# Kernel optimization log

Measured on AMD Instinct MI355X. Metric: run time of the kernel, lower is better.

## Reference

```python
import jax, jax.numpy as jnp
import numpy as np

B, S, H, D = 2, 4096, 16, 128
TILE = 128
T = S // TILE          # 32 tiles
TOPK = 7               # anchor-selected tiles per query tile (local tile appended -> 8)
DM = H * D
NEG = -1e10


def setup_inputs() -> dict:
    key = jax.random.key(0)
    ks = jax.random.split(key, 6)
    x = jax.random.normal(ks[0], (B, S, DM), dtype=jnp.float32)
    wq = jax.random.normal(ks[1], (DM, H * D), dtype=jnp.float32) * 0.02
    wk = jax.random.normal(ks[2], (DM, H * D), dtype=jnp.float32) * 0.02
    wv = jax.random.normal(ks[3], (DM, H * D), dtype=jnp.float32) * 0.02
    wo = jax.random.normal(ks[4], (H * D, DM), dtype=jnp.float32) * 0.02
    # RoPE tables (real/imag of freqs_cis), LLaMA-style
    inv_freq = 1.0 / (10000.0 ** (np.arange(0, D, 2, dtype=np.float32) / D))  # [D/2]
    t = np.arange(S, dtype=np.float32)
    freqs = np.outer(t, inv_freq)  # [S, D/2]
    cos = jnp.asarray(np.cos(freqs), dtype=jnp.float32)
    sin = jnp.asarray(np.sin(freqs), dtype=jnp.float32)
    anchor_indices = jax.random.randint(ks[5], (B, H, T, TOPK), 0, T, dtype=jnp.int32)
    return {"x": x, "wq": wq, "wk": wk, "wv": wv, "wo": wo,
            "cos": cos, "sin": sin, "anchor_indices": anchor_indices}


def _apply_rope(q, k, cos, sin):
    # q,k: [B,H,S,D]; cos,sin: [S,D/2]
    cos_f = jnp.concatenate([cos, cos], axis=-1)[None, None]  # [1,1,S,D]
    sin_f = jnp.concatenate([sin, sin], axis=-1)[None, None]

    def rot_half(x):
        h = x.shape[-1] // 2
        return jnp.concatenate([-x[..., h:], x[..., :h]], axis=-1)

    return q * cos_f + rot_half(q) * sin_f, k * cos_f + rot_half(k) * sin_f


def reference(x, wq, wk, wv, wo, cos, sin, anchor_indices):
    b, s, _ = x.shape
    h = anchor_indices.shape[1]
    t = anchor_indices.shape[2]
    tile = s // t
    d = wq.shape[1] // h

    q = (x @ wq).reshape(b, s, h, d).transpose(0, 2, 1, 3)  # [B,H,S,D]
    k = (x @ wk).reshape(b, s, h, d).transpose(0, 2, 1, 3)
    v = (x @ wv).reshape(b, s, h, d).transpose(0, 2, 1, 3)
    q, k = _apply_rope(q, k, cos, sin)

    # append local tile to anchor-selected tiles -> [B,H,T,K+1]
    local = jnp.broadcast_to(jnp.arange(t, dtype=jnp.int32)[None, None, :, None], (b, h, t, 1))
    tile_sel = jnp.concatenate([anchor_indices, local], axis=-1)
    # token indices of gathered tiles: [B,H,T,(K+1)*tile]
    offs = jnp.arange(tile, dtype=jnp.int32)[None, None, None, None, :]
    tok_idx = (tile_sel[..., None] * tile + offs)
    sparse_len = tile_sel.shape[-1] * tile
    flat_idx = jnp.clip(tok_idx.reshape(b, h, t, sparse_len), 0, s - 1)

    # gather K/V tiles: [B,H,T,L,D]
    gid = flat_idx.reshape(b, h, t * sparse_len)
    k_sp = jnp.take_along_axis(k, gid[..., None], axis=2).reshape(b, h, t, sparse_len, d)
    v_sp = jnp.take_along_axis(v, gid[..., None], axis=2).reshape(b, h, t, sparse_len, d)

    q_t = q.reshape(b, h, t, tile, d)
    logits = jnp.einsum('bhtqd,bhtkd->bhtqk', q_t, k_sp) / jnp.sqrt(jnp.float32(d))

    # causal future-mask within gathered set
    q_pos = jnp.arange(s, dtype=jnp.int32).reshape(t, tile)
    fut = flat_idx[:, :, :, None, :] > q_pos[None, None, :, :, None]  # [B,H,T,tile,L]
    logits = jnp.where(fut, NEG, logits)
    weights = jax.nn.softmax(logits, axis=-1)
    all_masked = jnp.all(fut, axis=-1, keepdims=True)
    weights = jnp.where(all_masked, 0.0, weights)
    weights = jnp.where(jnp.isnan(weights), 0.0, weights)

    out = jnp.einsum('bhtqk,bhtkd->bhtqd', weights, v_sp)
    out = out.reshape(b, h, s, d).transpose(0, 2, 1, 3).reshape(b, s, h * d)
    return out @ wo
```

## Files before the change

### kernel.cpp

```cpp
#include <hip/hip_runtime.h>
#include <hip/hip_bf16.h>


typedef __bf16 bf16_t;
using bf16x8 = __attribute__((ext_vector_type(8))) __bf16;
using bf16x4 = __attribute__((ext_vector_type(4))) __bf16;
using f32x4  = __attribute__((ext_vector_type(4))) float;

typedef const __attribute__((address_space(1))) void* gas_ptr;
typedef __attribute__((address_space(3))) void* las_ptr;

__device__ __forceinline__ void async_copy16(const void* g, void* l) {
  __builtin_amdgcn_global_load_lds((gas_ptr)g, (las_ptr)l, 16, 0, 0);
}

__device__ __forceinline__ f32x4 mfma16x16x32(bf16x8 a, bf16x8 b, f32x4 c) {
  return __builtin_amdgcn_mfma_f32_16x16x32_bf16(a, b, c, 0, 0, 0);
}

__global__ void cvt_f32_bf16(const float* __restrict__ X, bf16_t* __restrict__ Y) {
  int idx = blockIdx.x * 256 + threadIdx.x;
  float4 v = ((const float4*)X)[idx];
  bf16x4 r;
  r.x = (bf16_t)v.x; r.y = (bf16_t)v.y; r.z = (bf16_t)v.z; r.w = (bf16_t)v.w;
  ((bf16x4*)Y)[idx] = r;
}

__global__ void wtrans(const float* __restrict__ W, bf16_t* __restrict__ Wt) {
  __shared__ bf16_t t[64][66];
  const int r0 = blockIdx.x * 64, c0 = blockIdx.y * 64;
  const int tx = threadIdx.x & 63, ty = threadIdx.x >> 6;
  #pragma unroll
  for (int i = 0; i < 16; ++i) {
    int r = ty + 4 * i;
    t[r][tx] = (bf16_t)W[(size_t)(r0 + r) * 2048 + c0 + tx];
  }
  __syncthreads();
  #pragma unroll
  for (int i = 0; i < 16; ++i) {
    int n = ty + 4 * i;
    Wt[(size_t)(c0 + n) * 2048 + r0 + tx] = t[tx][n];
  }
}

__global__ __launch_bounds__(512, 2) void gemm256(
    const bf16_t* __restrict__ A, const bf16_t* __restrict__ Bt,
    int nb, int mode, float* __restrict__ Cf,
    bf16_t* __restrict__ outQ, bf16_t* __restrict__ outK,
    bf16_t* __restrict__ outVT,
    const float* __restrict__ cosT, const float* __restrict__ sinT)
{
  __shared__ bf16_t Apan[4][8192];
  __shared__ bf16_t Bpan[4][8192];
  const int bid = blockIdx.x;
  const int cpx = gridDim.x >> 3;
  const int swz = (bid & 7) * cpx + (bid >> 3);
  const int bm = (swz / nb) * 256, bn = (swz % nb) * 256;
  const int tid = threadIdx.x;
  const int w = tid >> 6, l = tid & 63;
  const int wr = w >> 1, wc = w & 1;
  const int fr = l & 15, g4 = l >> 4;

  const int c0 = tid, c1 = tid + 512;
  const int r0 = c0 >> 2, s0c = ((c0 & 3) ^ ((r0 >> 1) & 3)) * 8;
  const int r1 = c1 >> 2, s1c = ((c1 & 3) ^ ((r1 >> 1) & 3)) * 8;
  const bf16_t* aS0 = A  + (size_t)(bm + r0) * 2048 + s0c;
  const bf16_t* aS1 = A  + (size_t)(bm + r1) * 2048 + s1c;
  const bf16_t* bS0 = Bt + (size_t)(bn + r0) * 2048 + s0c;
  const bf16_t* bS1 = Bt + (size_t)(bn + r1) * 2048 + s1c;
  const int d0 = c0 * 16, d1 = c1 * 16;

  int aOff[4], bOff[8];
  #pragma unroll
  for (int m = 0; m < 4; ++m) {
    int R = wr * 64 + m * 16 + fr;
    aOff[m] = R * 64 + ((g4 ^ ((R >> 1) & 3)) << 4);
  }
  #pragma unroll
  for (int n = 0; n < 8; ++n) {
    int R = wc * 128 + n * 16 + fr;
    bOff[n] = R * 64 + ((g4 ^ ((R >> 1) & 3)) << 4);
  }

  f32x4 acc[4][8];
  #pragma unroll
  for (int m = 0; m < 4; ++m)
    #pragma unroll
    for (int n = 0; n < 8; ++n) acc[m][n] = (f32x4){0.f, 0.f, 0.f, 0.f};

  auto STAGE = [&](int phi2) {
    const int slot = phi2 & 3;
    const int kb = phi2 * 32;
    char* dA = (char*)&Apan[slot][0];
    char* dB = (char*)&Bpan[slot][0];
    async_copy16(aS0 + kb, dA + d0);
    async_copy16(aS1 + kb, dA + d1);
    async_copy16(bS0 + kb, dB + d0);
    async_copy16(bS1 + kb, dB + d1);
  };

  STAGE(0);
  STAGE(1);
  __syncthreads();

  #pragma unroll 1
  for (int phi = 0; phi < 64; ++phi) {
    const int slot = phi & 3;
    const char* pa = (const char*)&Apan[slot][0];
    const char* pb = (const char*)&Bpan[slot][0];
    bf16x8 af[4], bfr[8];
    #pragma unroll
    for (int m = 0; m < 4; ++m) af[m] = *(const bf16x8*)(pa + aOff[m]);
    #pragma unroll
    for (int n = 0; n < 8; ++n) bfr[n] = *(const bf16x8*)(pb + bOff[n]);
    if (phi < 62) {
      STAGE(phi + 2);
      asm volatile("s_waitcnt vmcnt(4)" ::: "memory");
    } else {
      asm volatile("s_waitcnt vmcnt(0)" ::: "memory");
    }
    __builtin_amdgcn_sched_barrier(0);
    __builtin_amdgcn_s_barrier();
    __builtin_amdgcn_sched_barrier(0);
    __builtin_amdgcn_s_setprio(1);
    #pragma unroll
    for (int m = 0; m < 4; ++m)
      #pragma unroll
      for (int n = 0; n < 8; ++n)
        acc[m][n] = mfma16x16x32(af[m], bfr[n], acc[m][n]);
    __builtin_amdgcn_s_setprio(0);
    __builtin_amdgcn_sched_barrier(0);
  }

  if (mode == 0) {
    #pragma unroll
    for (int m = 0; m < 4; ++m)
      #pragma unroll
      for (int n = 0; n < 8; ++n)
        #pragma unroll
        for (int j = 0; j < 4; ++j) {
          int row = bm + wr * 64 + m * 16 + g4 * 4 + j;
          int col = bn + wc * 128 + n * 16 + fr;
          Cf[(size_t)row * 2048 + col] = acc[m][n][j];
        }
    return;
  }

  const int colbase = bn + wc * 128;
  const int proj = colbase >> 11;
  const int hh = (colbase & 2047) >> 7;
  if (proj == 2) {
    #pragma unroll
    for (int m = 0; m < 4; ++m) {
      int row0 = bm + wr * 64 + m * 16 + g4 * 4;
      int b_ = row0 >> 12, sr = row0 & 4095;
      #pragma unroll
      for (int n = 0; n < 8; ++n) {
        int d_ = n * 16 + fr;
        bf16x4 pkv;
        #pragma unroll
        for (int j = 0; j < 4; ++j) pkv[j] = (bf16_t)acc[m][n][j];
        *(bf16x4*)&outVT[(((size_t)(b_ * 16 + hh)) * 128 + d_) * 4096 + sr] = pkv;
      }
    }
  } else {
    bf16_t* dst = proj ? outK : outQ;
    #pragma unroll
    for (int m = 0; m < 4; ++m) {
      int row0 = bm + wr * 64 + m * 16 + g4 * 4;
      int b_ = row0 >> 12, s0 = row0 & 4095;
      size_t hbase = ((size_t)(b_ * 16 + hh)) * 4096;
      #pragma unroll
      for (int n = 0; n < 4; ++n) {
        int d = n * 16 + fr;
        #pragma unroll
        for (int j = 0; j < 4; ++j) {
          int s = s0 + j;
          float c  = cosT[s * 64 + d];
          float sn = sinT[s * 64 + d];
          float x0 = acc[m][n][j], x1 = acc[m][n + 4][j];
          dst[(hbase + s) * 128 + d]      = (bf16_t)(x0 * c - x1 * sn);
          dst[(hbase + s) * 128 + d + 64] = (bf16_t)(x1 * c + x0 * sn);
        }
      }
    }
  }
}

__global__ __launch_bounds__(512, 4) void attn_kernel(
    const bf16_t* __restrict__ Qf, const bf16_t* __restrict__ Kf,
    const bf16_t* __restrict__ Vt, const int* __restrict__ anchors,
    bf16_t* __restrict__ outB)
{
  __shared__ bf16_t Kl[2][8192];
  __shared__ bf16_t Vl[2][8192];
  __shared__ bf16_t Pbuf[8][1024];
  const int orig = blockIdx.x;
  const int blk = (orig & 7) * 128 + (orig >> 3);
  const int qt = 31 - (blk & 31);
  const int h = (blk >> 5) & 15, b = blk >> 9;
  const int bh = b * 16 + h;
  const int tid = threadIdx.x, w = tid >> 6, l = tid & 63;
  const int fr = l & 15, g4 = l >> 4;
  const float scale = 0.08838834764831845f;

  const int* anc = anchors + ((size_t)bh * 32 + qt) * 7;
  unsigned long long pk = 0;
  int nt = 0;
  #pragma unroll
  for (int t = 0; t < 7; ++t) {
    int v = anc[t];
    if (v <= qt) { pk |= (unsigned long long)v << (5 * nt); ++nt; }
  }
  pk |= (unsigned long long)qt << (5 * nt); ++nt;
  const int NS = nt * 2;

  const bf16_t* Qbase = Qf + (size_t)bh * 4096 * 128;
  const bf16_t* Kbase = Kf + (size_t)bh * 4096 * 128;
  const bf16_t* Vbase = Vt + (size_t)bh * 128 * 4096;
  char* P = (char*)&Pbuf[w][0];

  auto STAGE = [&](int tb2, int p) {
    const bf16_t* ksrc = Kbase + (size_t)tb2 * 128;
    const bf16_t* vsrc = Vbase + tb2;
    char* kd = (char*)&Kl[p][0];
    char* vd = (char*)&Vl[p][0];
    #pragma unroll
    for (int i = 0; i < 2; ++i) {
      int c = tid + i * 512;
      int kr = c >> 4, kcol = c & 15;
      async_copy16(ksrc + (size_t)kr * 128 + (size_t)((kcol ^ (kr & 7)) * 8),
                   kd + c * 16);
      int vr = c >> 3, vcol = c & 7;
      async_copy16(vsrc + (size_t)vr * 4096 + (size_t)((vcol ^ (vr & 7)) * 8),
                   vd + c * 16);
    }
  };

  const int qrow = qt * 128 + w * 16 + fr;
  bf16x8 aq[4];
  #pragma unroll
  for (int kc = 0; kc < 4; ++kc)
    aq[kc] = *(const bf16x8*)(Qbase + (size_t)qrow * 128 + kc * 32 + g4 * 8);

  STAGE((int)(pk & 31) * 128, 0);
  __syncthreads();

  float mrun = -1e30f, lrun = 0.f;
  f32x4 o[8];
  #pragma unroll
  for (int nd = 0; nd < 8; ++nd) o[nd] = (f32x4){0.f, 0.f, 0.f, 0.f};

  for (int s = 0; s < NS; ++s) {
    const int p = s & 1;
    const int ts = (int)((pk >> (5 * (s >> 1))) & 31);
    const bool domask = (ts == qt);
    if (s + 1 < NS) {
      int s1 = s + 1;
      int ts1 = (int)((pk >> (5 * (s1 >> 1))) & 31);
      STAGE(ts1 * 128 + (s1 & 1) * 64, p ^ 1);
    }

    f32x4 sc[4];
    #pragma unroll
    for (int n = 0; n < 4; ++n) sc[n] = (f32x4){0.f, 0.f, 0.f, 0.f};
    #pragma unroll
    for (int kc = 0; kc < 4; ++kc) {
      bf16x8 kf[4];
      #pragma unroll
      for (int n = 0; n < 4; ++n) {
        int r = n * 16 + fr;
        kf[n] = *(const bf16x8*)((const char*)&Kl[p][0] +
                 r * 256 + (((kc * 4 + g4) ^ (r & 7)) << 4));
      }
      #pragma unroll
      for (int n = 0; n < 4; ++n)
        sc[n] = mfma16x16x32(kf[n], aq[kc], sc[n]);
    }

    float rmax = -1e30f;
    if (domask) {
      const int qr = w * 16 + fr;
      #pragma unroll
      for (int n = 0; n < 4; ++n)
        #pragma unroll
        for (int j = 0; j < 4; ++j) {
          float lg = sc[n][j] * scale;
          int tok = (s & 1) * 64 + n * 16 + g4 * 4 + j;
          if (tok > qr) lg = -1e10f;
          sc[n][j] = lg;
          rmax = fmaxf(rmax, lg);
        }
    } else {
      #pragma unroll
      for (int n = 0; n < 4; ++n)
        #pragma unroll
        for (int j = 0; j < 4; ++j) {
          float lg = sc[n][j] * scale;
          sc[n][j] = lg;
          rmax = fmaxf(rmax, lg);
        }
    }
    rmax = fmaxf(rmax, __shfl_xor(rmax, 16));
    rmax = fmaxf(rmax, __shfl_xor(rmax, 32));
    if (__any(rmax > mrun + 8.f)) {
      float mnew = fmaxf(mrun, rmax);
      float alpha = __expf(mrun - mnew);
      lrun *= alpha;
      #pragma unroll
      for (int nd = 0; nd < 8; ++nd)
        #pragma unroll
        for (int j = 0; j < 4; ++j) o[nd][j] *= alpha;
      mrun = mnew;
    }
    float rsum = 0.f;
    #pragma unroll
    for (int n = 0; n < 4; ++n) {
      bf16x4 pkv;
      #pragma unroll
      for (int j = 0; j < 4; ++j) {
        float pe = __expf(sc[n][j] - mrun);
        rsum += pe;
        pkv[j] = (bf16_t)pe;
      }
      int off = fr * 128 + ((((n << 1) | (g4 >> 1)) ^ (fr & 7)) << 4) + ((g4 & 1) << 3);
      *(bf16x4*)(P + off) = pkv;
    }
    rsum += __shfl_xor(rsum, 16);
    rsum += __shfl_xor(rsum, 32);
    lrun += rsum;

    #pragma unroll
    for (int kc2 = 0; kc2 < 2; ++kc2) {
      bf16x8 av[8];
      #pragma unroll
      for (int nd = 0; nd < 8; ++nd) {
        int r = nd * 16 + fr;
        av[nd] = *(const bf16x8*)((const char*)&Vl[p][0] +
                  r * 128 + (((kc2 * 4 + g4) ^ (r & 7)) << 4));
      }
      bf16x8 bp = *(const bf16x8*)(P + fr * 128 + ((((kc2 << 2) | g4) ^ (fr & 7)) << 4));
      #pragma unroll
      for (int nd = 0; nd < 8; ++nd)
        o[nd] = mfma16x16x32(av[nd], bp, o[nd]);
    }
    __syncthreads();
  }

  {
    char* E = (char*)&Kl[0][0] + w * 4096;
    float inv = 1.0f / lrun;
    #pragma unroll
    for (int nd = 0; nd < 8; ++nd) {
      bf16x4 pkv;
      #pragma unroll
      for (int j = 0; j < 4; ++j) pkv[j] = (bf16_t)(o[nd][j] * inv);
      int off = fr * 256 + ((((nd << 1) | (g4 >> 1)) ^ (fr & 7)) << 4) + ((g4 & 1) << 3);
      *(bf16x4*)(E + off) = pkv;
    }
    #pragma unroll
    for (int i = 0; i < 4; ++i) {
      int r = i * 4 + g4;
      int off = r * 256 + ((fr ^ (r & 7)) << 4);
      bf16x8 vrow = *(const bf16x8*)(E + off);
      size_t gaddr = (((size_t)b * 4096 + qt * 128 + w * 16 + r) * 2048)
                     + h * 128 + fr * 8;
      *(bf16x8*)(outB + gaddr) = vrow;
    }
  }
}

#define OFF_XB   ((size_t)0)
#define OFF_WCAT ((size_t)33554432)
#define OFF_WOT  ((size_t)58720256)
#define OFF_QF   ((size_t)67108864)
#define OFF_KF   ((size_t)100663296)
#define OFF_AT   ((size_t)134217728)
#define OFF_VT   ((size_t)167772160)

extern "C" void kernel_launch(void* const* d_in, const int* in_sizes, int n_in,
                              void* d_out, int out_size, void* d_ws, size_t ws_size,
                              hipStream_t stream) {
  (void)in_sizes; (void)n_in; (void)out_size; (void)ws_size;
  const float* x    = (const float*)d_in[0];
  const float* wq   = (const float*)d_in[1];
  const float* wk   = (const float*)d_in[2];
  const float* wv   = (const float*)d_in[3];
  const float* wo   = (const float*)d_in[4];
  const float* cosT = (const float*)d_in[5];
  const float* sinT = (const float*)d_in[6];
  const int*   anc  = (const int*)d_in[7];
  float* out = (float*)d_out;
  char* ws = (char*)d_ws;

  bf16_t* xb   = (bf16_t*)(ws + OFF_XB);
  bf16_t* wcat = (bf16_t*)(ws + OFF_WCAT);
  bf16_t* wqt  = wcat;
  bf16_t* wkt  = wcat + (size_t)2048 * 2048;
  bf16_t* wvt  = wcat + (size_t)4096 * 2048;
  bf16_t* wot  = (bf16_t*)(ws + OFF_WOT);
  bf16_t* Qf   = (bf16_t*)(ws + OFF_QF);
  bf16_t* Kf   = (bf16_t*)(ws + OFF_KF);
  bf16_t* Vt   = (bf16_t*)(ws + OFF_VT);
  bf16_t* attnB = (bf16_t*)(ws + OFF_AT);

  cvt_f32_bf16<<<16384, 256, 0, stream>>>(x, xb);
  wtrans<<<dim3(32, 32), 256, 0, stream>>>(wq, wqt);
  wtrans<<<dim3(32, 32), 256, 0, stream>>>(wk, wkt);
  wtrans<<<dim3(32, 32), 256, 0, stream>>>(wv, wvt);
  wtrans<<<dim3(32, 32), 256, 0, stream>>>(wo, wot);
  gemm256<<<768, 512, 0, stream>>>(xb, wcat, 24, 1, nullptr, Qf, Kf, Vt, cosT, sinT);
  attn_kernel<<<1024, 512, 0, stream>>>(Qf, Kf, Vt, anc, attnB);
  gemm256<<<256, 512, 0, stream>>>(attnB, wot, 8, 0, out, nullptr, nullptr, nullptr,
                                   nullptr, nullptr);
}
```

Baseline: 382.4 us.

## Split GEMM k-step into four sub-phases interleaving loads, async copies and MFMAs

Each k-iteration of the GEMM main loop is split into four sub-phases. Each sub-phase loads two B fragments, issues one of the four async global-to-LDS copies and runs 8 MFMAs. The aim is to spread LDS reads and global loads across the MFMA work, cut register pressure from holding eight B fragments, and overlap memory with compute more finely. In exchange it adds three extra workgroup barriers per iteration, and the prologue now waits only on the first stage instead of doing a full sync.

```diff
diff --git a/kernel.cpp b/kernel.cpp
--- a/kernel.cpp
+++ b/kernel.cpp
@@ -88,48 +88,55 @@
     #pragma unroll
     for (int n = 0; n < 8; ++n) acc[m][n] = (f32x4){0.f, 0.f, 0.f, 0.f};
 
-  auto STAGE = [&](int phi2) {
+  auto STAGE1 = [&](int phi2, int q) {
     const int slot = phi2 & 3;
     const int kb = phi2 * 32;
-    char* dA = (char*)&Apan[slot][0];
-    char* dB = (char*)&Bpan[slot][0];
-    async_copy16(aS0 + kb, dA + d0);
-    async_copy16(aS1 + kb, dA + d1);
-    async_copy16(bS0 + kb, dB + d0);
-    async_copy16(bS1 + kb, dB + d1);
+    if (q == 0)      async_copy16(aS0 + kb, (char*)&Apan[slot][0] + d0);
+    else if (q == 1) async_copy16(aS1 + kb, (char*)&Apan[slot][0] + d1);
+    else if (q == 2) async_copy16(bS0 + kb, (char*)&Bpan[slot][0] + d0);
+    else             async_copy16(bS1 + kb, (char*)&Bpan[slot][0] + d1);
   };
 
-  STAGE(0);
-  STAGE(1);
-  __syncthreads();
+  #pragma unroll
+  for (int q = 0; q < 4; ++q) STAGE1(0, q);
+  #pragma unroll
+  for (int q = 0; q < 4; ++q) STAGE1(1, q);
+  asm volatile("s_waitcnt vmcnt(4)" ::: "memory");
+  __builtin_amdgcn_sched_barrier(0);
+  __builtin_amdgcn_s_barrier();
+  __builtin_amdgcn_sched_barrier(0);
 
   #pragma unroll 1
   for (int phi = 0; phi < 64; ++phi) {
     const int slot = phi & 3;
     const char* pa = (const char*)&Apan[slot][0];
     const char* pb = (const char*)&Bpan[slot][0];
-    bf16x8 af[4], bfr[8];
-    #pragma unroll
-    for (int m = 0; m < 4; ++m) af[m] = *(const bf16x8*)(pa + aOff[m]);
-    #pragma unroll
-    for (int n = 0; n < 8; ++n) bfr[n] = *(const bf16x8*)(pb + bOff[n]);
-    if (phi < 62) {
-      STAGE(phi + 2);
-      asm volatile("s_waitcnt vmcnt(4)" ::: "memory");
-    } else {
-      asm volatile("s_waitcnt vmcnt(0)" ::: "memory");
-    }
-    __builtin_amdgcn_sched_barrier(0);
-    __builtin_amdgcn_s_barrier();
-    __builtin_amdgcn_sched_barrier(0);
-    __builtin_amdgcn_s_setprio(1);
-    #pragma unroll
-    for (int m = 0; m < 4; ++m)
-      #pragma unroll
-      for (int n = 0; n < 8; ++n)
-        acc[m][n] = mfma16x16x32(af[m], bfr[n], acc[m][n]);
-    __builtin_amdgcn_s_setprio(0);
-    __builtin_amdgcn_sched_barrier(0);
+    bf16x8 af[4];
+    #pragma unroll
+    for (int q = 0; q < 4; ++q) {
+      if (q == 0) {
+        #pragma unroll
+        for (int m = 0; m < 4; ++m) af[m] = *(const bf16x8*)(pa + aOff[m]);
+      }
+      bf16x8 b0 = *(const bf16x8*)(pb + bOff[2 * q]);
+      bf16x8 b1 = *(const bf16x8*)(pb + bOff[2 * q + 1]);
+      if (phi < 62) STAGE1(phi + 2, q);
+      if (q == 3) {
+        if (phi < 62) asm volatile("s_waitcnt vmcnt(4)" ::: "memory");
+        else          asm volatile("s_waitcnt vmcnt(0)" ::: "memory");
+      }
+      __builtin_amdgcn_sched_barrier(0);
+      __builtin_amdgcn_s_barrier();
+      __builtin_amdgcn_sched_barrier(0);
+      __builtin_amdgcn_s_setprio(1);
+      #pragma unroll
+      for (int m = 0; m < 4; ++m) {
+        acc[m][2 * q]     = mfma16x16x32(af[m], b0, acc[m][2 * q]);
+        acc[m][2 * q + 1] = mfma16x16x32(af[m], b1, acc[m][2 * q + 1]);
+      }
+      __builtin_amdgcn_s_setprio(0);
+      __builtin_amdgcn_sched_barrier(0);
+    }
   }
 
   if (mode == 0) {
```

Result: slower. 409.6 us (+7.1%).

## Restructure GEMM K-loop to 64-wide double-buffered stages with one barrier each

Applied to the files above, without the earlier changes.

The GEMM main loop now stages 64-wide K slices into two LDS buffers instead of 32-wide slices into four, with a matching 8-chunk XOR swizzle. Each iteration runs two MFMA sub-steps between barriers, halving barrier count per K. The prefetch depth drops from two stages ahead to one, and each iteration waits on vmcnt(0) after compute. This may expose more global-load latency.

```diff
diff --git a/kernel.cpp b/kernel.cpp
--- a/kernel.cpp
+++ b/kernel.cpp
@@ -50,8 +50,8 @@
     bf16_t* __restrict__ outVT,
     const float* __restrict__ cosT, const float* __restrict__ sinT)
 {
-  __shared__ bf16_t Apan[4][8192];
-  __shared__ bf16_t Bpan[4][8192];
+  __shared__ bf16_t Apan[2][16384];
+  __shared__ bf16_t Bpan[2][16384];
   const int bid = blockIdx.x;
   const int cpx = gridDim.x >> 3;
   const int swz = (bid & 7) * cpx + (bid >> 3);
@@ -61,25 +61,32 @@
   const int wr = w >> 1, wc = w & 1;
   const int fr = l & 15, g4 = l >> 4;
 
-  const int c0 = tid, c1 = tid + 512;
-  const int r0 = c0 >> 2, s0c = ((c0 & 3) ^ ((r0 >> 1) & 3)) * 8;
-  const int r1 = c1 >> 2, s1c = ((c1 & 3) ^ ((r1 >> 1) & 3)) * 8;
-  const bf16_t* aS0 = A  + (size_t)(bm + r0) * 2048 + s0c;
-  const bf16_t* aS1 = A  + (size_t)(bm + r1) * 2048 + s1c;
-  const bf16_t* bS0 = Bt + (size_t)(bn + r0) * 2048 + s0c;
-  const bf16_t* bS1 = Bt + (size_t)(bn + r1) * 2048 + s1c;
-  const int d0 = c0 * 16, d1 = c1 * 16;
-
-  int aOff[4], bOff[8];
-  #pragma unroll
-  for (int m = 0; m < 4; ++m) {
-    int R = wr * 64 + m * 16 + fr;
-    aOff[m] = R * 64 + ((g4 ^ ((R >> 1) & 3)) << 4);
-  }
-  #pragma unroll
-  for (int n = 0; n < 8; ++n) {
-    int R = wc * 128 + n * 16 + fr;
-    bOff[n] = R * 64 + ((g4 ^ ((R >> 1) & 3)) << 4);
+  const bf16_t* aS[4];
+  const bf16_t* bS[4];
+  int dst[4];
+  #pragma unroll
+  for (int i = 0; i < 4; ++i) {
+    int c = tid + i * 512;
+    int row = c >> 3, ch = c & 7;
+    int sc = (ch ^ (row & 7)) * 8;
+    aS[i] = A  + (size_t)(bm + row) * 2048 + sc;
+    bS[i] = Bt + (size_t)(bn + row) * 2048 + sc;
+    dst[i] = c * 16;
+  }
+
+  int aOff[2][4], bOff[2][8];
+  #pragma unroll
+  for (int kc = 0; kc < 2; ++kc) {
+    #pragma unroll
+    for (int m = 0; m < 4; ++m) {
+      int R = wr * 64 + m * 16 + fr;
+      aOff[kc][m] = R * 128 + (((kc * 4 + g4) ^ (R & 7)) << 4);
+    }
+    #pragma unroll
+    for (int n = 0; n < 8; ++n) {
+      int R = wc * 128 + n * 16 + fr;
+      bOff[kc][n] = R * 128 + (((kc * 4 + g4) ^ (R & 7)) << 4);
+    }
   }
 
   f32x4 acc[4][8];
@@ -88,47 +95,57 @@
     #pragma unroll
     for (int n = 0; n < 8; ++n) acc[m][n] = (f32x4){0.f, 0.f, 0.f, 0.f};
 
-  auto STAGE = [&](int phi2) {
-    const int slot = phi2 & 3;
-    const int kb = phi2 * 32;
+  auto STAGE = [&](int t) {
+    const int slot = t & 1;
+    const int kb = t * 64;
     char* dA = (char*)&Apan[slot][0];
     char* dB = (char*)&Bpan[slot][0];
-    async_copy16(aS0 + kb, dA + d0);
-    async_copy16(aS1 + kb, dA + d1);
-    async_copy16(bS0 + kb, dB + d0);
-    async_copy16(bS1 + kb, dB + d1);
+    #pragma unroll
+    for (int i = 0; i < 4; ++i) {
+      async_copy16(aS[i] + kb, dA + dst[i]);
+      async_copy16(bS[i] + kb, dB + dst[i]);
+    }
   };
 
   STAGE(0);
-  STAGE(1);
   __syncthreads();
 
   #pragma unroll 1
-  for (int phi = 0; phi < 64; ++phi) {
-    const int slot = phi & 3;
+  for (int phi = 0; phi < 32; ++phi) {
+    const int slot = phi & 1;
     const char* pa = (const char*)&Apan[slot][0];
     const char* pb = (const char*)&Bpan[slot][0];
-    bf16x8 af[4], bfr[8];
-    #pragma unroll
-    for (int m = 0; m < 4; ++m) af[m] = *(const bf16x8*)(pa + aOff[m]);
-    #pragma unroll
-    for (int n = 0; n < 8; ++n) bfr[n] = *(const bf16x8*)(pb + bOff[n]);
-    if (phi < 62) {
-      STAGE(phi + 2);
-      asm volatile("s_waitcnt vmcnt(4)" ::: "memory");
-    } else {
-      asm volatile("s_waitcnt vmcnt(0)" ::: "memory");
-    }
+
+    bf16x8 af0[4], bf0[8];
+    #pragma unroll
+    for (int m = 0; m < 4; ++m) af0[m] = *(const bf16x8*)(pa + aOff[0][m]);
+    #pragma unroll
+    for (int n = 0; n < 8; ++n) bf0[n] = *(const bf16x8*)(pb + bOff[0][n]);
+    if (phi < 31) STAGE(phi + 1);
+    __builtin_amdgcn_s_setprio(1);
+    #pragma unroll
+    for (int m = 0; m < 4; ++m)
+      #pragma unroll
+      for (int n = 0; n < 8; ++n)
+        acc[m][n] = mfma16x16x32(af0[m], bf0[n], acc[m][n]);
+    __builtin_amdgcn_s_setprio(0);
+
+    bf16x8 af1[4], bf1[8];
+    #pragma unroll
+    for (int m = 0; m < 4; ++m) af1[m] = *(const bf16x8*)(pa + aOff[1][m]);
+    #pragma unroll
+    for (int n = 0; n < 8; ++n) bf1[n] = *(const bf16x8*)(pb + bOff[1][n]);
+    __builtin_amdgcn_s_setprio(1);
+    #pragma unroll
+    for (int m = 0; m < 4; ++m)
+      #pragma unroll
+      for (int n = 0; n < 8; ++n)
+        acc[m][n] = mfma16x16x32(af1[m], bf1[n], acc[m][n]);
+    __builtin_amdgcn_s_setprio(0);
+
+    asm volatile("s_waitcnt vmcnt(0)" ::: "memory");
     __builtin_amdgcn_sched_barrier(0);
     __builtin_amdgcn_s_barrier();
-    __builtin_amdgcn_sched_barrier(0);
-    __builtin_amdgcn_s_setprio(1);
-    #pragma unroll
-    for (int m = 0; m < 4; ++m)
-      #pragma unroll
-      for (int n = 0; n < 8; ++n)
-        acc[m][n] = mfma16x16x32(af[m], bfr[n], acc[m][n]);
-    __builtin_amdgcn_s_setprio(0);
     __builtin_amdgcn_sched_barrier(0);
   }
 
@@ -164,7 +181,7 @@
       }
     }
   } else {
-    bf16_t* dst = proj ? outK : outQ;
+    bf16_t* dst_ = proj ? outK : outQ;
     #pragma unroll
     for (int m = 0; m < 4; ++m) {
       int row0 = bm + wr * 64 + m * 16 + g4 * 4;
@@ -179,8 +196,8 @@
           float c  = cosT[s * 64 + d];
           float sn = sinT[s * 64 + d];
           float x0 = acc[m][n][j], x1 = acc[m][n + 4][j];
-          dst[(hbase + s) * 128 + d]      = (bf16_t)(x0 * c - x1 * sn);
-          dst[(hbase + s) * 128 + d + 64] = (bf16_t)(x1 * c + x0 * sn);
+          dst_[(hbase + s) * 128 + d]      = (bf16_t)(x0 * c - x1 * sn);
+          dst_[(hbase + s) * 128 + d + 64] = (bf16_t)(x1 * c + x0 * sn);
         }
       }
     }
```

New measurement: 369.3 us. 1.04x faster.

## Shrink GEMM tile to 128x256 with 3-stage pipeline and merge weight transposes

Applied to the files above, without the earlier changes.

Replaces the 256x256, 512-thread GEMM with a 128x256, 256-thread variant that uses a 3-slot LDS ring and one barrier per iteration placed after the MFMAs. The idea is to double the block count so the QKV and output projections fill the CUs better, with less LDS per block. It also fuses the four weight-transpose launches into one z-indexed launch to cut launch overhead. Smaller M tiles lower reuse of the B panel and raise global traffic per FLOP.

```diff
diff --git a/kernel.cpp b/kernel.cpp
--- a/kernel.cpp
+++ b/kernel.cpp
@@ -26,8 +26,13 @@
   ((bf16x4*)Y)[idx] = r;
 }
 
-__global__ void wtrans(const float* __restrict__ W, bf16_t* __restrict__ Wt) {
+__global__ void wtrans4(const float* __restrict__ wq, const float* __restrict__ wk,
+                        const float* __restrict__ wv, const float* __restrict__ wo,
+                        bf16_t* __restrict__ wcat, bf16_t* __restrict__ wot) {
   __shared__ bf16_t t[64][66];
+  const int z = blockIdx.z;
+  const float* W = (z == 0) ? wq : (z == 1) ? wk : (z == 2) ? wv : wo;
+  bf16_t* Wt = (z == 3) ? wot : (wcat + (size_t)z * 2048 * 2048);
   const int r0 = blockIdx.x * 64, c0 = blockIdx.y * 64;
   const int tx = threadIdx.x & 63, ty = threadIdx.x >> 6;
   #pragma unroll
@@ -43,32 +48,41 @@
   }
 }
 
-__global__ __launch_bounds__(512, 2) void gemm256(
+__global__ __launch_bounds__(256, 2) void gemm128(
     const bf16_t* __restrict__ A, const bf16_t* __restrict__ Bt,
     int nb, int mode, float* __restrict__ Cf,
     bf16_t* __restrict__ outQ, bf16_t* __restrict__ outK,
     bf16_t* __restrict__ outVT,
     const float* __restrict__ cosT, const float* __restrict__ sinT)
 {
-  __shared__ bf16_t Apan[4][8192];
-  __shared__ bf16_t Bpan[4][8192];
+  __shared__ bf16_t Apan[3][4096];
+  __shared__ bf16_t Bpan[3][8192];
   const int bid = blockIdx.x;
   const int cpx = gridDim.x >> 3;
   const int swz = (bid & 7) * cpx + (bid >> 3);
-  const int bm = (swz / nb) * 256, bn = (swz % nb) * 256;
+  const int bm = (swz / nb) * 128, bn = (swz % nb) * 256;
   const int tid = threadIdx.x;
   const int w = tid >> 6, l = tid & 63;
   const int wr = w >> 1, wc = w & 1;
   const int fr = l & 15, g4 = l >> 4;
 
-  const int c0 = tid, c1 = tid + 512;
-  const int r0 = c0 >> 2, s0c = ((c0 & 3) ^ ((r0 >> 1) & 3)) * 8;
-  const int r1 = c1 >> 2, s1c = ((c1 & 3) ^ ((r1 >> 1) & 3)) * 8;
-  const bf16_t* aS0 = A  + (size_t)(bm + r0) * 2048 + s0c;
-  const bf16_t* aS1 = A  + (size_t)(bm + r1) * 2048 + s1c;
-  const bf16_t* bS0 = Bt + (size_t)(bn + r0) * 2048 + s0c;
-  const bf16_t* bS1 = Bt + (size_t)(bn + r1) * 2048 + s1c;
-  const int d0 = c0 * 16, d1 = c1 * 16;
+  const bf16_t* aS[2];
+  const bf16_t* bS[4];
+  int dA[2], dB[4];
+  #pragma unroll
+  for (int i = 0; i < 2; ++i) {
+    int c = tid + i * 256;
+    int row = c >> 2, ch = c & 3;
+    aS[i] = A + (size_t)(bm + row) * 2048 + (ch ^ ((row >> 1) & 3)) * 8;
+    dA[i] = c * 16;
+  }
+  #pragma unroll
+  for (int i = 0; i < 4; ++i) {
+    int c = tid + i * 256;
+    int row = c >> 2, ch = c & 3;
+    bS[i] = Bt + (size_t)(bn + row) * 2048 + (ch ^ ((row >> 1) & 3)) * 8;
+    dB[i] = c * 16;
+  }
 
   int aOff[4], bOff[8];
   #pragma unroll
@@ -88,40 +102,35 @@
     #pragma unroll
     for (int n = 0; n < 8; ++n) acc[m][n] = (f32x4){0.f, 0.f, 0.f, 0.f};
 
-  auto STAGE = [&](int phi2) {
-    const int slot = phi2 & 3;
-    const int kb = phi2 * 32;
-    char* dA = (char*)&Apan[slot][0];
-    char* dB = (char*)&Bpan[slot][0];
-    async_copy16(aS0 + kb, dA + d0);
-    async_copy16(aS1 + kb, dA + d1);
-    async_copy16(bS0 + kb, dB + d0);
-    async_copy16(bS1 + kb, dB + d1);
+  auto STAGE = [&](int t) {
+    const int slot = t % 3;
+    const int kb = t * 32;
+    char* pA = (char*)&Apan[slot][0];
+    char* pB = (char*)&Bpan[slot][0];
+    #pragma unroll
+    for (int i = 0; i < 2; ++i) async_copy16(aS[i] + kb, pA + dA[i]);
+    #pragma unroll
+    for (int i = 0; i < 4; ++i) async_copy16(bS[i] + kb, pB + dB[i]);
   };
 
   STAGE(0);
   STAGE(1);
-  __syncthreads();
+  asm volatile("s_waitcnt vmcnt(6)" ::: "memory");
+  __builtin_amdgcn_sched_barrier(0);
+  __builtin_amdgcn_s_barrier();
+  __builtin_amdgcn_sched_barrier(0);
 
   #pragma unroll 1
   for (int phi = 0; phi < 64; ++phi) {
-    const int slot = phi & 3;
+    const int slot = phi % 3;
     const char* pa = (const char*)&Apan[slot][0];
     const char* pb = (const char*)&Bpan[slot][0];
+    if (phi < 62) STAGE(phi + 2);
     bf16x8 af[4], bfr[8];
     #pragma unroll
     for (int m = 0; m < 4; ++m) af[m] = *(const bf16x8*)(pa + aOff[m]);
     #pragma unroll
     for (int n = 0; n < 8; ++n) bfr[n] = *(const bf16x8*)(pb + bOff[n]);
-    if (phi < 62) {
-      STAGE(phi + 2);
-      asm volatile("s_waitcnt vmcnt(4)" ::: "memory");
-    } else {
-      asm volatile("s_waitcnt vmcnt(0)" ::: "memory");
-    }
-    __builtin_amdgcn_sched_barrier(0);
-    __builtin_amdgcn_s_barrier();
-    __builtin_amdgcn_sched_barrier(0);
     __builtin_amdgcn_s_setprio(1);
     #pragma unroll
     for (int m = 0; m < 4; ++m)
@@ -129,6 +138,10 @@
       for (int n = 0; n < 8; ++n)
         acc[m][n] = mfma16x16x32(af[m], bfr[n], acc[m][n]);
     __builtin_amdgcn_s_setprio(0);
+    if (phi < 62) asm volatile("s_waitcnt vmcnt(6)" ::: "memory");
+    else          asm volatile("s_waitcnt vmcnt(0)" ::: "memory");
+    __builtin_amdgcn_sched_barrier(0);
+    __builtin_amdgcn_s_barrier();
     __builtin_amdgcn_sched_barrier(0);
   }
 
@@ -164,7 +177,7 @@
       }
     }
   } else {
-    bf16_t* dst = proj ? outK : outQ;
+    bf16_t* dst_ = proj ? outK : outQ;
     #pragma unroll
     for (int m = 0; m < 4; ++m) {
       int row0 = bm + wr * 64 + m * 16 + g4 * 4;
@@ -179,8 +192,8 @@
           float c  = cosT[s * 64 + d];
           float sn = sinT[s * 64 + d];
           float x0 = acc[m][n][j], x1 = acc[m][n + 4][j];
-          dst[(hbase + s) * 128 + d]      = (bf16_t)(x0 * c - x1 * sn);
-          dst[(hbase + s) * 128 + d + 64] = (bf16_t)(x1 * c + x0 * sn);
+          dst_[(hbase + s) * 128 + d]      = (bf16_t)(x0 * c - x1 * sn);
+          dst_[(hbase + s) * 128 + d + 64] = (bf16_t)(x1 * c + x0 * sn);
         }
       }
     }
@@ -395,9 +408,6 @@
 
   bf16_t* xb   = (bf16_t*)(ws + OFF_XB);
   bf16_t* wcat = (bf16_t*)(ws + OFF_WCAT);
-  bf16_t* wqt  = wcat;
-  bf16_t* wkt  = wcat + (size_t)2048 * 2048;
-  bf16_t* wvt  = wcat + (size_t)4096 * 2048;
   bf16_t* wot  = (bf16_t*)(ws + OFF_WOT);
   bf16_t* Qf   = (bf16_t*)(ws + OFF_QF);
   bf16_t* Kf   = (bf16_t*)(ws + OFF_KF);
@@ -405,12 +415,9 @@
   bf16_t* attnB = (bf16_t*)(ws + OFF_AT);
 
   cvt_f32_bf16<<<16384, 256, 0, stream>>>(x, xb);
-  wtrans<<<dim3(32, 32), 256, 0, stream>>>(wq, wqt);
-  wtrans<<<dim3(32, 32), 256, 0, stream>>>(wk, wkt);
-  wtrans<<<dim3(32, 32), 256, 0, stream>>>(wv, wvt);
-  wtrans<<<dim3(32, 32), 256, 0, stream>>>(wo, wot);
-  gemm256<<<768, 512, 0, stream>>>(xb, wcat, 24, 1, nullptr, Qf, Kf, Vt, cosT, sinT);
+  wtrans4<<<dim3(32, 32, 4), 256, 0, stream>>>(wq, wk, wv, wo, wcat, wot);
+  gemm128<<<1536, 256, 0, stream>>>(xb, wcat, 24, 1, nullptr, Qf, Kf, Vt, cosT, sinT);
   attn_kernel<<<1024, 512, 0, stream>>>(Qf, Kf, Vt, anc, attnB);
-  gemm256<<<256, 512, 0, stream>>>(attnB, wot, 8, 0, out, nullptr, nullptr, nullptr,
+  gemm128<<<512, 256, 0, stream>>>(attnB, wot, 8, 0, out, nullptr, nullptr, nullptr,
                                    nullptr, nullptr);
 }
```

Result: slower. 425.4 us (+11.2%).
